# Kernel tuning notes

Measured on AMD Instinct MI355X. Metric: run time of the kernel, lower is better.

## Reference

```python
import jax, jax.numpy as jnp
import numpy as np

B, C, H, W = 256, 3, 224, 224
RETINA = 32
NUM_ZOOM = 3
SCALE = 2
HG, HL = 1024, 256  # num_hidden_glimpse, num_hidden_location
GDIM = NUM_ZOOM * C * RETINA * RETINA  # 9216


def setup_inputs() -> dict:
    key = jax.random.key(0)
    ks = jax.random.split(key, 12)
    images = jax.random.normal(ks[0], (B, C, H, W), dtype=jnp.float32)
    # locations in [-0.4, 0.4] so all multi-scale crops are in-bounds
    locations = (jax.random.uniform(ks[1], (B, 2), dtype=jnp.float32) * 2.0 - 1.0) * 0.4
    def lin(kw, kb, fan_in, fan_out):
        s = 1.0 / np.sqrt(fan_in)
        Wm = jax.random.uniform(kw, (fan_in, fan_out), jnp.float32, -s, s)
        bm = jax.random.uniform(kb, (fan_out,), jnp.float32, -s, s)
        return Wm, bm
    W1, b1 = lin(ks[2], ks[3], GDIM, HG)
    W2, b2 = lin(ks[4], ks[5], 2, HL)
    W3, b3 = lin(ks[6], ks[7], HG, HG + HL)
    W4, b4 = lin(ks[8], ks[9], HL, HG + HL)
    return {"images": images, "locations": locations,
            "W1": W1, "b1": b1, "W2": W2, "b2": b2,
            "W3": W3, "b3": b3, "W4": W4, "b4": b4}


def _foveate(images, locations):
    # images (B,C,H,W); locations (B,2) in [-1,1]
    denorm = (locations + 1.0) * 0.5 * W  # denormalized pixel coords (row, col)
    zoom_patches = []
    for i in range(NUM_ZOOM):
        half = int(RETINA * 0.5 * SCALE ** i)
        size = 2 * half
        def crop(img, loc):
            # int() truncation == floor for in-bounds (non-negative) offsets
            top = jnp.trunc(loc[0] - half).astype(jnp.int32)
            left = jnp.trunc(loc[1] - half).astype(jnp.int32)
            return jax.lax.dynamic_slice(img, (jnp.int32(0), top, left), (C, size, size))
        crops = jax.vmap(crop)(images, denorm)  # (B,C,size,size)
        resized = jax.image.resize(crops, (crops.shape[0], C, RETINA, RETINA),
                                   method="bilinear", antialias=False)
        zoom_patches.append(resized)
    g = jnp.stack(zoom_patches, axis=1)  # (B, Z, C, r, r)
    return g.reshape(g.shape[0], -1)  # (B, Z*C*r*r)


def reference(images, locations, W1, b1, W2, b2, W3, b3, W4, b4):
    g = _foveate(images, locations)
    hg = jax.nn.relu(jax.nn.relu(g @ W1 + b1) @ W3 + b3)
    hl = jax.nn.relu(jax.nn.relu(locations @ W2 + b2) @ W4 + b4)
    return jax.nn.relu(hg + hl)
```

## Files before the change

kernel.cpp:

```cpp
#include <hip/hip_runtime.h>

typedef __attribute__((ext_vector_type(8))) short short8;
typedef __attribute__((ext_vector_type(4))) float f32x4;

#define Bsz 256
#define Cch 3
#define Him 224
#define Wim 224
#define RET 32
#define HG 1024
#define HL 256
#define GDIM 9216
#define NOUT 1280

__device__ __forceinline__ unsigned short f2bf(float x) {
  unsigned u = __float_as_uint(x);
  unsigned r = (u + 0x7fffu + ((u >> 16) & 1u)) >> 16;
  return (unsigned short)r;
}
__device__ __forceinline__ float bf2f(unsigned short h) {
  return __uint_as_float((unsigned)h << 16);
}

#define GLL(gp, lp)                                                        \
  __builtin_amdgcn_global_load_lds(                                        \
      (const __attribute__((address_space(1))) unsigned int*)(gp),         \
      (__attribute__((address_space(3))) unsigned int*)(lp), 16, 0, 0)

__global__ __launch_bounds__(256) void foveate_kernel(
    const float* __restrict__ img, const float* __restrict__ loc,
    unsigned short* __restrict__ ghi, unsigned short* __restrict__ glo) {
  int q = blockIdx.x * 256 + threadIdx.x;
  int idx = q * 4;
  int b = idx / GDIM;
  int r = idx - b * GDIM;
  int z = r / (Cch * RET * RET);
  int r2 = r - z * (Cch * RET * RET);
  int c = r2 / (RET * RET);
  int p = r2 - c * (RET * RET);
  int i = p >> 5, j0 = p & 31;
  float dr = (loc[b * 2 + 0] + 1.f) * .5f * (float)Wim;
  float dc = (loc[b * 2 + 1] + 1.f) * .5f * (float)Wim;
  int half = 16 << z;
  int top = (int)truncf(dr - (float)half), left = (int)truncf(dc - (float)half);
  const float* base = img + ((long)b * Cch + c) * (Him * Wim);
  float v[4];
  if (z == 0) {
    const float* rp = base + (top + i) * Wim + left + j0;
#pragma unroll
    for (int t = 0; t < 4; ++t) v[t] = rp[t];
  } else if (z == 1) {
    const float* rp = base + (top + 2 * i) * Wim + left + 2 * j0;
#pragma unroll
    for (int t = 0; t < 4; ++t)
      v[t] = .25f * (rp[2 * t] + rp[2 * t + 1] + rp[Wim + 2 * t] + rp[Wim + 2 * t + 1]);
  } else {
    const float* rp = base + (top + 4 * i + 1) * Wim + left + 4 * j0 + 1;
#pragma unroll
    for (int t = 0; t < 4; ++t)
      v[t] = .25f * (rp[4 * t] + rp[4 * t + 1] + rp[Wim + 4 * t] + rp[Wim + 4 * t + 1]);
  }
  unsigned short h0 = f2bf(v[0]), h1 = f2bf(v[1]), h2 = f2bf(v[2]), h3 = f2bf(v[3]);
  *(ushort4*)(ghi + idx) = make_ushort4(h0, h1, h2, h3);
  *(ushort4*)(glo + idx) =
      make_ushort4(f2bf(v[0] - bf2f(h0)), f2bf(v[1] - bf2f(h1)),
                   f2bf(v[2] - bf2f(h2)), f2bf(v[3] - bf2f(h3)));
}

__global__ __launch_bounds__(256) void tconv_kernel(
    const float* __restrict__ in, unsigned short* __restrict__ oh,
    unsigned short* __restrict__ ol, int K, int N) {
  __shared__ float tile[32][33];
  int n0 = blockIdx.x * 32, k0 = blockIdx.y * 32;
  int r = threadIdx.x >> 3, c4 = (threadIdx.x & 7) * 4;
  float4 v = *(const float4*)(in + (long)(k0 + r) * N + n0 + c4);
  tile[r][c4 + 0] = v.x; tile[r][c4 + 1] = v.y;
  tile[r][c4 + 2] = v.z; tile[r][c4 + 3] = v.w;
  __syncthreads();
  float x0 = tile[c4 + 0][r], x1 = tile[c4 + 1][r];
  float x2 = tile[c4 + 2][r], x3 = tile[c4 + 3][r];
  unsigned short h0 = f2bf(x0), h1 = f2bf(x1), h2 = f2bf(x2), h3 = f2bf(x3);
  long o = (long)(n0 + r) * K + k0 + c4;
  *(ushort4*)(oh + o) = make_ushort4(h0, h1, h2, h3);
  *(ushort4*)(ol + o) = make_ushort4(f2bf(x0 - bf2f(h0)), f2bf(x1 - bf2f(h1)),
                                     f2bf(x2 - bf2f(h2)), f2bf(x3 - bf2f(h3)));
}

__device__ __forceinline__ void mfma_tile(
    const unsigned short* __restrict__ Ahi, const unsigned short* __restrict__ Alo, int lda,
    const unsigned short* __restrict__ Bhi, const unsigned short* __restrict__ Blo, int ldb,
    int m0, int n0, int kb, int iters, f32x4 acc[4][4], unsigned short* lds) {
  const int t = threadIdx.x;
  const int lane = t & 63;
  const int wid = t >> 6;
  const int wm = (t >> 7) & 1, wn = (t >> 6) & 1;
  unsigned short* pAh = lds;
  unsigned short* pAl = lds + 4096;
  unsigned short* pBh = lds + 8192;
  unsigned short* pBl = lds + 12288;
  const int c0 = 2 * wid, c1 = 2 * wid + 1;
  const int sr = lane & 15, sk = (lane >> 4) * 8;
  const long a0 = (long)(m0 + c0 * 16 + sr) * lda + kb + sk;
  const long a1 = (long)(m0 + c1 * 16 + sr) * lda + kb + sk;
  const long b0 = (long)(n0 + c0 * 16 + sr) * ldb + kb + sk;
  const long b1 = (long)(n0 + c1 * 16 + sr) * ldb + kb + sk;
  const int l0 = c0 * 512, l1 = c1 * 512;

  for (int it = 0; it < iters; ++it) {
    const long ka = (long)it * 32;
    __syncthreads();
    GLL(Ahi + a0 + ka, pAh + l0);
    GLL(Ahi + a1 + ka, pAh + l1);
    GLL(Alo + a0 + ka, pAl + l0);
    GLL(Alo + a1 + ka, pAl + l1);
    GLL(Bhi + b0 + ka, pBh + l0);
    GLL(Bhi + b1 + ka, pBh + l1);
    GLL(Blo + b0 + ka, pBl + l0);
    GLL(Blo + b1 + ka, pBl + l1);
    __syncthreads();
    short8 ah[4], al[4], bh[4], bl[4];
#pragma unroll
    for (int f = 0; f < 4; ++f) {
      int ra = ((wm * 4 + f) * 64 + lane) * 8;
      int rb = ((wn * 4 + f) * 64 + lane) * 8;
      ah[f] = *(const short8*)(pAh + ra);
      al[f] = *(const short8*)(pAl + ra);
      bh[f] = *(const short8*)(pBh + rb);
      bl[f] = *(const short8*)(pBl + rb);
    }
#pragma unroll
    for (int mf = 0; mf < 4; ++mf)
#pragma unroll
      for (int nf = 0; nf < 4; ++nf) {
        acc[mf][nf] = __builtin_amdgcn_mfma_f32_16x16x32_bf16(ah[mf], bh[nf], acc[mf][nf], 0, 0, 0);
        acc[mf][nf] = __builtin_amdgcn_mfma_f32_16x16x32_bf16(ah[mf], bl[nf], acc[mf][nf], 0, 0, 0);
        acc[mf][nf] = __builtin_amdgcn_mfma_f32_16x16x32_bf16(al[mf], bh[nf], acc[mf][nf], 0, 0, 0);
      }
  }
}

__device__ __forceinline__ void epilogue(float* __restrict__ Pz, int ldp, int m0, int n0,
                                         f32x4 acc[4][4]) {
  const int t = threadIdx.x, lane = t & 63;
  const int wm = (t >> 7) & 1, wn = (t >> 6) & 1;
  const int rbase = (lane >> 4) * 4, col = lane & 15;
#pragma unroll
  for (int mf = 0; mf < 4; ++mf)
#pragma unroll
    for (int nf = 0; nf < 4; ++nf) {
      int row = m0 + wm * 64 + mf * 16 + rbase;
      int cc = n0 + wn * 64 + nf * 16 + col;
#pragma unroll
      for (int r = 0; r < 4; ++r)
        Pz[(long)(row + r) * ldp + cc] = acc[mf][nf][r];
    }
}

__global__ __launch_bounds__(256, 2) void gemm1_kernel(
    const unsigned short* __restrict__ ghi, const unsigned short* __restrict__ glo,
    const unsigned short* __restrict__ w1thi, const unsigned short* __restrict__ w1tlo,
    float* __restrict__ P) {
  __shared__ __align__(16) unsigned short lds[16384];
  f32x4 zz = {0.f, 0.f, 0.f, 0.f};
  f32x4 acc[4][4];
  for (int i = 0; i < 4; ++i) for (int j = 0; j < 4; ++j) acc[i][j] = zz;
  int n0 = blockIdx.x * 128, m0 = blockIdx.y * 128, z = blockIdx.z;
  mfma_tile(ghi, glo, GDIM, w1thi, w1tlo, GDIM, m0, n0, z * 288, 9, acc, lds);
  epilogue(P + (long)z * Bsz * HG, HG, m0, n0, acc);
}

__global__ __launch_bounds__(256, 2) void gemm2_kernel(
    const unsigned short* __restrict__ h1hi, const unsigned short* __restrict__ h1lo,
    const unsigned short* __restrict__ h2hi, const unsigned short* __restrict__ h2lo,
    const unsigned short* __restrict__ w3thi, const unsigned short* __restrict__ w3tlo,
    const unsigned short* __restrict__ w4thi, const unsigned short* __restrict__ w4tlo,
    float* __restrict__ P) {
  __shared__ __align__(16) unsigned short lds[16384];
  f32x4 zz = {0.f, 0.f, 0.f, 0.f};
  f32x4 acc[4][4];
  for (int i = 0; i < 4; ++i) for (int j = 0; j < 4; ++j) acc[i][j] = zz;
  int n0 = blockIdx.x * 128, m0 = blockIdx.y * 128, z = blockIdx.z;
  if (z < 8)
    mfma_tile(h1hi, h1lo, HG, w3thi, w3tlo, HG, m0, n0, z * 128, 4, acc, lds);
  else
    mfma_tile(h2hi, h2lo, HL, w4thi, w4tlo, HL, m0, n0, (z - 8) * 128, 4, acc, lds);
  epilogue(P + (long)z * Bsz * NOUT, NOUT, m0, n0, acc);
}

__global__ __launch_bounds__(256) void reduce1_kernel(
    const float* __restrict__ P, const float* __restrict__ b1,
    unsigned short* __restrict__ h1hi, unsigned short* __restrict__ h1lo) {
  int i4 = (blockIdx.x * 256 + threadIdx.x) * 4;
  float4 s = *(const float4*)(P + i4);
  for (int z = 1; z < 32; ++z) {
    float4 p = *(const float4*)(P + (long)z * (Bsz * HG) + i4);
    s.x += p.x; s.y += p.y; s.z += p.z; s.w += p.w;
  }
  int n = i4 & (HG - 1);
  float4 bb = *(const float4*)(b1 + n);
  float v0 = fmaxf(s.x + bb.x, 0.f), v1 = fmaxf(s.y + bb.y, 0.f);
  float v2 = fmaxf(s.z + bb.z, 0.f), v3 = fmaxf(s.w + bb.w, 0.f);
  unsigned short h0 = f2bf(v0), h1 = f2bf(v1), h2 = f2bf(v2), h3 = f2bf(v3);
  *(ushort4*)(h1hi + i4) = make_ushort4(h0, h1, h2, h3);
  *(ushort4*)(h1lo + i4) = make_ushort4(f2bf(v0 - bf2f(h0)), f2bf(v1 - bf2f(h1)),
                                        f2bf(v2 - bf2f(h2)), f2bf(v3 - bf2f(h3)));
}

__global__ __launch_bounds__(256) void h2_kernel(
    const float* __restrict__ loc, const float* __restrict__ W2,
    const float* __restrict__ b2, unsigned short* __restrict__ h2hi,
    unsigned short* __restrict__ h2lo) {
  int b = blockIdx.x, n = threadIdx.x;
  float s = fmaf(loc[b * 2], W2[n], fmaf(loc[b * 2 + 1], W2[HL + n], b2[n]));
  s = fmaxf(s, 0.f);
  unsigned short h = f2bf(s);
  h2hi[b * HL + n] = h;
  h2lo[b * HL + n] = f2bf(s - bf2f(h));
}

__global__ __launch_bounds__(256) void reduce2_kernel(
    const float* __restrict__ P, const float* __restrict__ b3,
    const float* __restrict__ b4, float* __restrict__ out) {
  int i4 = (blockIdx.x * 256 + threadIdx.x) * 4;
  float4 a = *(const float4*)(P + i4);
  for (int z = 1; z < 8; ++z) {
    float4 p = *(const float4*)(P + (long)z * (Bsz * NOUT) + i4);
    a.x += p.x; a.y += p.y; a.z += p.z; a.w += p.w;
  }
  float4 c0 = *(const float4*)(P + 8L * (Bsz * NOUT) + i4);
  float4 c1 = *(const float4*)(P + 9L * (Bsz * NOUT) + i4);
  float4 c;
  c.x = c0.x + c1.x; c.y = c0.y + c1.y; c.z = c0.z + c1.z; c.w = c0.w + c1.w;
  int n = i4 % NOUT;
  float4 b3v = *(const float4*)(b3 + n);
  float4 b4v = *(const float4*)(b4 + n);
  float4 o;
  o.x = fmaxf(fmaxf(a.x + b3v.x, 0.f) + fmaxf(c.x + b4v.x, 0.f), 0.f);
  o.y = fmaxf(fmaxf(a.y + b3v.y, 0.f) + fmaxf(c.y + b4v.y, 0.f), 0.f);
  o.z = fmaxf(fmaxf(a.z + b3v.z, 0.f) + fmaxf(c.z + b4v.z, 0.f), 0.f);
  o.w = fmaxf(fmaxf(a.w + b3v.w, 0.f) + fmaxf(c.w + b4v.w, 0.f), 0.f);
  *(float4*)(out + i4) = o;
}

extern "C" void kernel_launch(void* const* d_in, const int* in_sizes, int n_in,
                              void* d_out, int out_size, void* d_ws, size_t ws_size,
                              hipStream_t stream) {
  const float* images = (const float*)d_in[0];
  const float* locs = (const float*)d_in[1];
  const float* W1 = (const float*)d_in[2];
  const float* b1 = (const float*)d_in[3];
  const float* W2 = (const float*)d_in[4];
  const float* b2 = (const float*)d_in[5];
  const float* W3 = (const float*)d_in[6];
  const float* b3 = (const float*)d_in[7];
  const float* W4 = (const float*)d_in[8];
  const float* b4 = (const float*)d_in[9];
  float* out = (float*)d_out;

  unsigned short* ghi = (unsigned short*)d_ws;
  unsigned short* glo = ghi + (long)Bsz * GDIM;
  unsigned short* w1thi = glo + (long)Bsz * GDIM;
  unsigned short* w1tlo = w1thi + (long)GDIM * HG;
  unsigned short* w3thi = w1tlo + (long)GDIM * HG;
  unsigned short* w3tlo = w3thi + (long)HG * NOUT;
  unsigned short* w4thi = w3tlo + (long)HG * NOUT;
  unsigned short* w4tlo = w4thi + (long)HL * NOUT;
  unsigned short* h1hi = w4tlo + (long)HL * NOUT;
  unsigned short* h1lo = h1hi + (long)Bsz * HG;
  unsigned short* h2hi = h1lo + (long)Bsz * HG;
  unsigned short* h2lo = h2hi + (long)Bsz * HL;
  float* P1 = (float*)(h2lo + (long)Bsz * HL);
  float* P2 = P1;

  tconv_kernel<<<dim3(HG / 32, GDIM / 32), 256, 0, stream>>>(W1, w1thi, w1tlo, GDIM, HG);
  tconv_kernel<<<dim3(NOUT / 32, HG / 32), 256, 0, stream>>>(W3, w3thi, w3tlo, HG, NOUT);
  tconv_kernel<<<dim3(NOUT / 32, HL / 32), 256, 0, stream>>>(W4, w4thi, w4tlo, HL, NOUT);
  foveate_kernel<<<(Bsz * GDIM) / 1024, 256, 0, stream>>>(images, locs, ghi, glo);
  gemm1_kernel<<<dim3(HG / 128, Bsz / 128, 32), 256, 0, stream>>>(ghi, glo, w1thi, w1tlo, P1);
  reduce1_kernel<<<(Bsz * HG) / 1024, 256, 0, stream>>>(P1, b1, h1hi, h1lo);
  h2_kernel<<<Bsz, HL, 0, stream>>>(locs, W2, b2, h2hi, h2lo);
  gemm2_kernel<<<dim3(NOUT / 128, Bsz / 128, 10), 256, 0, stream>>>(
      h1hi, h1lo, h2hi, h2lo, w3thi, w3tlo, w4thi, w4tlo, P2);
  reduce2_kernel<<<(Bsz * NOUT) / 1024, 256, 0, stream>>>(P2, b3, b4, out);
}
```

Baseline: 295.7 us.

## Double-buffer GEMM LDS loads and merge prep/reduce kernels to cut launches

The MFMA tile loop now double-buffers LDS, so the next K-slice's global-to-LDS loads are issued before computing on the current slice, with a single waitcnt+barrier per iteration. Separately, the foveate and three weight-transpose kernels are merged into one prep launch, and reduce1 and h2 are merged into one launch, to cut launch overhead and tail gaps. LDS per block doubles to 64KB, which may limit occupancy below the requested two blocks per CU.

```diff
diff --git a/kernel.cpp b/kernel.cpp
--- a/kernel.cpp
+++ b/kernel.cpp
@@ -27,51 +27,73 @@
       (const __attribute__((address_space(1))) unsigned int*)(gp),         \
       (__attribute__((address_space(3))) unsigned int*)(lp), 16, 0, 0)
 
-__global__ __launch_bounds__(256) void foveate_kernel(
+#define WAIT_BAR() asm volatile("s_waitcnt vmcnt(0)\n\ts_barrier" ::: "memory")
+
+__global__ __launch_bounds__(256) void prep_kernel(
     const float* __restrict__ img, const float* __restrict__ loc,
-    unsigned short* __restrict__ ghi, unsigned short* __restrict__ glo) {
-  int q = blockIdx.x * 256 + threadIdx.x;
-  int idx = q * 4;
-  int b = idx / GDIM;
-  int r = idx - b * GDIM;
-  int z = r / (Cch * RET * RET);
-  int r2 = r - z * (Cch * RET * RET);
-  int c = r2 / (RET * RET);
-  int p = r2 - c * (RET * RET);
-  int i = p >> 5, j0 = p & 31;
-  float dr = (loc[b * 2 + 0] + 1.f) * .5f * (float)Wim;
-  float dc = (loc[b * 2 + 1] + 1.f) * .5f * (float)Wim;
-  int half = 16 << z;
-  int top = (int)truncf(dr - (float)half), left = (int)truncf(dc - (float)half);
-  const float* base = img + ((long)b * Cch + c) * (Him * Wim);
-  float v[4];
-  if (z == 0) {
-    const float* rp = base + (top + i) * Wim + left + j0;
-#pragma unroll
-    for (int t = 0; t < 4; ++t) v[t] = rp[t];
-  } else if (z == 1) {
-    const float* rp = base + (top + 2 * i) * Wim + left + 2 * j0;
-#pragma unroll
-    for (int t = 0; t < 4; ++t)
-      v[t] = .25f * (rp[2 * t] + rp[2 * t + 1] + rp[Wim + 2 * t] + rp[Wim + 2 * t + 1]);
+    unsigned short* __restrict__ ghi, unsigned short* __restrict__ glo,
+    const float* __restrict__ W1, unsigned short* __restrict__ w1thi,
+    unsigned short* __restrict__ w1tlo, const float* __restrict__ W3,
+    unsigned short* __restrict__ w3thi, unsigned short* __restrict__ w3tlo,
+    const float* __restrict__ W4, unsigned short* __restrict__ w4thi,
+    unsigned short* __restrict__ w4tlo) {
+  int id = blockIdx.x;
+  if (id < 2304) {
+    int q = id * 256 + threadIdx.x;
+    int idx = q * 4;
+    int b = idx / GDIM;
+    int r = idx - b * GDIM;
+    int z = r / (Cch * RET * RET);
+    int r2 = r - z * (Cch * RET * RET);
+    int c = r2 / (RET * RET);
+    int p = r2 - c * (RET * RET);
+    int i = p >> 5, j0 = p & 31;
+    float dr = (loc[b * 2 + 0] + 1.f) * .5f * (float)Wim;
+    float dc = (loc[b * 2 + 1] + 1.f) * .5f * (float)Wim;
+    int half = 16 << z;
+    int top = (int)truncf(dr - (float)half), left = (int)truncf(dc - (float)half);
+    const float* base = img + ((long)b * Cch + c) * (Him * Wim);
+    float v[4];
+    if (z == 0) {
+      const float* rp = base + (top + i) * Wim + left + j0;
+#pragma unroll
+      for (int t = 0; t < 4; ++t) v[t] = rp[t];
+    } else if (z == 1) {
+      const float* rp = base + (top + 2 * i) * Wim + left + 2 * j0;
+#pragma unroll
+      for (int t = 0; t < 4; ++t)
+        v[t] = .25f * (rp[2 * t] + rp[2 * t + 1] + rp[Wim + 2 * t] + rp[Wim + 2 * t + 1]);
+    } else {
+      const float* rp = base + (top + 4 * i + 1) * Wim + left + 4 * j0 + 1;
+#pragma unroll
+      for (int t = 0; t < 4; ++t)
+        v[t] = .25f * (rp[4 * t] + rp[4 * t + 1] + rp[Wim + 4 * t] + rp[Wim + 4 * t + 1]);
+    }
+    unsigned short h0 = f2bf(v[0]), h1 = f2bf(v[1]), h2 = f2bf(v[2]), h3 = f2bf(v[3]);
+    *(ushort4*)(ghi + idx) = make_ushort4(h0, h1, h2, h3);
+    *(ushort4*)(glo + idx) =
+        make_ushort4(f2bf(v[0] - bf2f(h0)), f2bf(v[1] - bf2f(h1)),
+                     f2bf(v[2] - bf2f(h2)), f2bf(v[3] - bf2f(h3)));
+    return;
+  }
+  id -= 2304;
+  const float* in;
+  unsigned short *oh, *ol;
+  int K, N, bx, by;
+  if (id < 9216) {
+    in = W1; oh = w1thi; ol = w1tlo; K = GDIM; N = HG;
+    bx = id & 31; by = id >> 5;
+  } else if (id < 10496) {
+    id -= 9216;
+    in = W3; oh = w3thi; ol = w3tlo; K = HG; N = NOUT;
+    bx = id % 40; by = id / 40;
   } else {
-    const float* rp = base + (top + 4 * i + 1) * Wim + left + 4 * j0 + 1;
-#pragma unroll
-    for (int t = 0; t < 4; ++t)
-      v[t] = .25f * (rp[4 * t] + rp[4 * t + 1] + rp[Wim + 4 * t] + rp[Wim + 4 * t + 1]);
-  }
-  unsigned short h0 = f2bf(v[0]), h1 = f2bf(v[1]), h2 = f2bf(v[2]), h3 = f2bf(v[3]);
-  *(ushort4*)(ghi + idx) = make_ushort4(h0, h1, h2, h3);
-  *(ushort4*)(glo + idx) =
-      make_ushort4(f2bf(v[0] - bf2f(h0)), f2bf(v[1] - bf2f(h1)),
-                   f2bf(v[2] - bf2f(h2)), f2bf(v[3] - bf2f(h3)));
-}
-
-__global__ __launch_bounds__(256) void tconv_kernel(
-    const float* __restrict__ in, unsigned short* __restrict__ oh,
-    unsigned short* __restrict__ ol, int K, int N) {
+    id -= 10496;
+    in = W4; oh = w4thi; ol = w4tlo; K = HL; N = NOUT;
+    bx = id % 40; by = id / 40;
+  }
   __shared__ float tile[32][33];
-  int n0 = blockIdx.x * 32, k0 = blockIdx.y * 32;
+  int n0 = bx * 32, k0 = by * 32;
   int r = threadIdx.x >> 3, c4 = (threadIdx.x & 7) * 4;
   float4 v = *(const float4*)(in + (long)(k0 + r) * N + n0 + c4);
   tile[r][c4 + 0] = v.x; tile[r][c4 + 1] = v.y;
@@ -94,10 +116,6 @@
   const int lane = t & 63;
   const int wid = t >> 6;
   const int wm = (t >> 7) & 1, wn = (t >> 6) & 1;
-  unsigned short* pAh = lds;
-  unsigned short* pAl = lds + 4096;
-  unsigned short* pBh = lds + 8192;
-  unsigned short* pBl = lds + 12288;
   const int c0 = 2 * wid, c1 = 2 * wid + 1;
   const int sr = lane & 15, sk = (lane >> 4) * 8;
   const long a0 = (long)(m0 + c0 * 16 + sr) * lda + kb + sk;
@@ -106,27 +124,35 @@
   const long b1 = (long)(n0 + c1 * 16 + sr) * ldb + kb + sk;
   const int l0 = c0 * 512, l1 = c1 * 512;
 
+#define STAGE(buf, tt)                                                     \
+  do {                                                                     \
+    unsigned short* L_ = lds + (buf) * 16384;                              \
+    const long ka_ = (long)(tt) * 32;                                      \
+    GLL(Ahi + a0 + ka_, L_ + l0);                                          \
+    GLL(Ahi + a1 + ka_, L_ + l1);                                          \
+    GLL(Alo + a0 + ka_, L_ + 4096 + l0);                                   \
+    GLL(Alo + a1 + ka_, L_ + 4096 + l1);                                   \
+    GLL(Bhi + b0 + ka_, L_ + 8192 + l0);                                   \
+    GLL(Bhi + b1 + ka_, L_ + 8192 + l1);                                   \
+    GLL(Blo + b0 + ka_, L_ + 12288 + l0);                                  \
+    GLL(Blo + b1 + ka_, L_ + 12288 + l1);                                  \
+  } while (0)
+
+  STAGE(0, 0);
+  WAIT_BAR();
+  int cur = 0;
   for (int it = 0; it < iters; ++it) {
-    const long ka = (long)it * 32;
-    __syncthreads();
-    GLL(Ahi + a0 + ka, pAh + l0);
-    GLL(Ahi + a1 + ka, pAh + l1);
-    GLL(Alo + a0 + ka, pAl + l0);
-    GLL(Alo + a1 + ka, pAl + l1);
-    GLL(Bhi + b0 + ka, pBh + l0);
-    GLL(Bhi + b1 + ka, pBh + l1);
-    GLL(Blo + b0 + ka, pBl + l0);
-    GLL(Blo + b1 + ka, pBl + l1);
-    __syncthreads();
+    if (it + 1 < iters) STAGE(cur ^ 1, it + 1);
+    unsigned short* L = lds + cur * 16384;
     short8 ah[4], al[4], bh[4], bl[4];
 #pragma unroll
     for (int f = 0; f < 4; ++f) {
       int ra = ((wm * 4 + f) * 64 + lane) * 8;
       int rb = ((wn * 4 + f) * 64 + lane) * 8;
-      ah[f] = *(const short8*)(pAh + ra);
-      al[f] = *(const short8*)(pAl + ra);
-      bh[f] = *(const short8*)(pBh + rb);
-      bl[f] = *(const short8*)(pBl + rb);
+      ah[f] = *(const short8*)(L + ra);
+      al[f] = *(const short8*)(L + 4096 + ra);
+      bh[f] = *(const short8*)(L + 8192 + rb);
+      bl[f] = *(const short8*)(L + 12288 + rb);
     }
 #pragma unroll
     for (int mf = 0; mf < 4; ++mf)
@@ -136,7 +162,10 @@
         acc[mf][nf] = __builtin_amdgcn_mfma_f32_16x16x32_bf16(ah[mf], bl[nf], acc[mf][nf], 0, 0, 0);
         acc[mf][nf] = __builtin_amdgcn_mfma_f32_16x16x32_bf16(al[mf], bh[nf], acc[mf][nf], 0, 0, 0);
       }
-  }
+    WAIT_BAR();
+    cur ^= 1;
+  }
+#undef STAGE
 }
 
 __device__ __forceinline__ void epilogue(float* __restrict__ Pz, int ldp, int m0, int n0,
@@ -160,7 +189,7 @@
     const unsigned short* __restrict__ ghi, const unsigned short* __restrict__ glo,
     const unsigned short* __restrict__ w1thi, const unsigned short* __restrict__ w1tlo,
     float* __restrict__ P) {
-  __shared__ __align__(16) unsigned short lds[16384];
+  __shared__ __align__(16) unsigned short lds[32768];
   f32x4 zz = {0.f, 0.f, 0.f, 0.f};
   f32x4 acc[4][4];
   for (int i = 0; i < 4; ++i) for (int j = 0; j < 4; ++j) acc[i][j] = zz;
@@ -175,7 +204,7 @@
     const unsigned short* __restrict__ w3thi, const unsigned short* __restrict__ w3tlo,
     const unsigned short* __restrict__ w4thi, const unsigned short* __restrict__ w4tlo,
     float* __restrict__ P) {
-  __shared__ __align__(16) unsigned short lds[16384];
+  __shared__ __align__(16) unsigned short lds[32768];
   f32x4 zz = {0.f, 0.f, 0.f, 0.f};
   f32x4 acc[4][4];
   for (int i = 0; i < 4; ++i) for (int j = 0; j < 4; ++j) acc[i][j] = zz;
@@ -187,35 +216,35 @@
   epilogue(P + (long)z * Bsz * NOUT, NOUT, m0, n0, acc);
 }
 
-__global__ __launch_bounds__(256) void reduce1_kernel(
+__global__ __launch_bounds__(256) void reduce1h2_kernel(
     const float* __restrict__ P, const float* __restrict__ b1,
-    unsigned short* __restrict__ h1hi, unsigned short* __restrict__ h1lo) {
-  int i4 = (blockIdx.x * 256 + threadIdx.x) * 4;
-  float4 s = *(const float4*)(P + i4);
-  for (int z = 1; z < 32; ++z) {
-    float4 p = *(const float4*)(P + (long)z * (Bsz * HG) + i4);
-    s.x += p.x; s.y += p.y; s.z += p.z; s.w += p.w;
-  }
-  int n = i4 & (HG - 1);
-  float4 bb = *(const float4*)(b1 + n);
-  float v0 = fmaxf(s.x + bb.x, 0.f), v1 = fmaxf(s.y + bb.y, 0.f);
-  float v2 = fmaxf(s.z + bb.z, 0.f), v3 = fmaxf(s.w + bb.w, 0.f);
-  unsigned short h0 = f2bf(v0), h1 = f2bf(v1), h2 = f2bf(v2), h3 = f2bf(v3);
-  *(ushort4*)(h1hi + i4) = make_ushort4(h0, h1, h2, h3);
-  *(ushort4*)(h1lo + i4) = make_ushort4(f2bf(v0 - bf2f(h0)), f2bf(v1 - bf2f(h1)),
-                                        f2bf(v2 - bf2f(h2)), f2bf(v3 - bf2f(h3)));
-}
-
-__global__ __launch_bounds__(256) void h2_kernel(
+    unsigned short* __restrict__ h1hi, unsigned short* __restrict__ h1lo,
     const float* __restrict__ loc, const float* __restrict__ W2,
     const float* __restrict__ b2, unsigned short* __restrict__ h2hi,
     unsigned short* __restrict__ h2lo) {
-  int b = blockIdx.x, n = threadIdx.x;
-  float s = fmaf(loc[b * 2], W2[n], fmaf(loc[b * 2 + 1], W2[HL + n], b2[n]));
-  s = fmaxf(s, 0.f);
-  unsigned short h = f2bf(s);
-  h2hi[b * HL + n] = h;
-  h2lo[b * HL + n] = f2bf(s - bf2f(h));
+  if (blockIdx.x < 256) {
+    int i4 = (blockIdx.x * 256 + threadIdx.x) * 4;
+    float4 s = *(const float4*)(P + i4);
+    for (int z = 1; z < 32; ++z) {
+      float4 p = *(const float4*)(P + (long)z * (Bsz * HG) + i4);
+      s.x += p.x; s.y += p.y; s.z += p.z; s.w += p.w;
+    }
+    int n = i4 & (HG - 1);
+    float4 bb = *(const float4*)(b1 + n);
+    float v0 = fmaxf(s.x + bb.x, 0.f), v1 = fmaxf(s.y + bb.y, 0.f);
+    float v2 = fmaxf(s.z + bb.z, 0.f), v3 = fmaxf(s.w + bb.w, 0.f);
+    unsigned short h0 = f2bf(v0), h1 = f2bf(v1), h2 = f2bf(v2), h3 = f2bf(v3);
+    *(ushort4*)(h1hi + i4) = make_ushort4(h0, h1, h2, h3);
+    *(ushort4*)(h1lo + i4) = make_ushort4(f2bf(v0 - bf2f(h0)), f2bf(v1 - bf2f(h1)),
+                                          f2bf(v2 - bf2f(h2)), f2bf(v3 - bf2f(h3)));
+  } else {
+    int b = blockIdx.x - 256, n = threadIdx.x;
+    float s = fmaf(loc[b * 2], W2[n], fmaf(loc[b * 2 + 1], W2[HL + n], b2[n]));
+    s = fmaxf(s, 0.f);
+    unsigned short h = f2bf(s);
+    h2hi[b * HL + n] = h;
+    h2lo[b * HL + n] = f2bf(s - bf2f(h));
+  }
 }
 
 __global__ __launch_bounds__(256) void reduce2_kernel(
@@ -272,13 +301,10 @@
   float* P1 = (float*)(h2lo + (long)Bsz * HL);
   float* P2 = P1;
 
-  tconv_kernel<<<dim3(HG / 32, GDIM / 32), 256, 0, stream>>>(W1, w1thi, w1tlo, GDIM, HG);
-  tconv_kernel<<<dim3(NOUT / 32, HG / 32), 256, 0, stream>>>(W3, w3thi, w3tlo, HG, NOUT);
-  tconv_kernel<<<dim3(NOUT / 32, HL / 32), 256, 0, stream>>>(W4, w4thi, w4tlo, HL, NOUT);
-  foveate_kernel<<<(Bsz * GDIM) / 1024, 256, 0, stream>>>(images, locs, ghi, glo);
+  prep_kernel<<<13120, 256, 0, stream>>>(images, locs, ghi, glo, W1, w1thi, w1tlo,
+                                         W3, w3thi, w3tlo, W4, w4thi, w4tlo);
   gemm1_kernel<<<dim3(HG / 128, Bsz / 128, 32), 256, 0, stream>>>(ghi, glo, w1thi, w1tlo, P1);
-  reduce1_kernel<<<(Bsz * HG) / 1024, 256, 0, stream>>>(P1, b1, h1hi, h1lo);
-  h2_kernel<<<Bsz, HL, 0, stream>>>(locs, W2, b2, h2hi, h2lo);
+  reduce1h2_kernel<<<512, 256, 0, stream>>>(P1, b1, h1hi, h1lo, locs, W2, b2, h2hi, h2lo);
   gemm2_kernel<<<dim3(NOUT / 128, Bsz / 128, 10), 256, 0, stream>>>(
       h1hi, h1lo, h2hi, h2lo, w3thi, w3tlo, w4thi, w4tlo, P2);
   reduce2_kernel<<<(Bsz * NOUT) / 1024, 256, 0, stream>>>(P2, b3, b4, out);
```

Result: faster. 289.1 us (-2.2%).
